# Performance work log

Hardware: AMD Instinct MI355X
Metric: run time of the kernel (lower is better)

Reference implementation:

```python
import jax, jax.numpy as jnp
import numpy as np

NOTES = 51
EMBED = 50
HID = 25
B, T = 512, 2048


def _lstm_layer(x_seq, Wih, Whh, bih, bhh):
    """x_seq: [T, B, in]; returns (ys [T,B,H], h_n [B,H], c_n [B,H]).
    PyTorch gate order: i, f, g, o."""
    H = Whh.shape[1]
    Bsz = x_seq.shape[1]
    # Precompute input projection for all timesteps (one big GEMM).
    xz = jnp.einsum('tbi,gi->tbg', x_seq, Wih) + bih + bhh  # [T, B, 4H]

    def step(carry, xz_t):
        h, c = carry
        z = xz_t + h @ Whh.T  # [B, 4H]
        i, f, g, o = jnp.split(z, 4, axis=-1)
        c = jax.nn.sigmoid(f) * c + jax.nn.sigmoid(i) * jnp.tanh(g)
        h = jax.nn.sigmoid(o) * jnp.tanh(c)
        return (h, c), h

    init = (jnp.zeros((Bsz, H), x_seq.dtype), jnp.zeros((Bsz, H), x_seq.dtype))
    (h_n, c_n), ys = jax.lax.scan(step, init, xz)
    return ys, h_n, c_n


def setup_inputs() -> dict:
    key = jax.random.key(0)
    ks = jax.random.split(key, 12)
    s = 0.1
    inp = {
        'x': jax.random.randint(ks[0], (B, T), 0, NOTES, dtype=jnp.int32),
        'emb': jax.random.normal(ks[1], (NOTES, EMBED), jnp.float32) * s,
        'Wih0': jax.random.normal(ks[2], (4 * HID, EMBED), jnp.float32) * s,
        'Whh0': jax.random.normal(ks[3], (4 * HID, HID), jnp.float32) * s,
        'bih0': jax.random.normal(ks[4], (4 * HID,), jnp.float32) * s,
        'bhh0': jax.random.normal(ks[5], (4 * HID,), jnp.float32) * s,
        'Wih1': jax.random.normal(ks[6], (4 * HID, HID), jnp.float32) * s,
        'Whh1': jax.random.normal(ks[7], (4 * HID, HID), jnp.float32) * s,
        'bih1': jax.random.normal(ks[8], (4 * HID,), jnp.float32) * s,
        'bhh1': jax.random.normal(ks[9], (4 * HID,), jnp.float32) * s,
        'fcW': jax.random.normal(ks[10], (NOTES, HID), jnp.float32) * s,
        'fcb': jax.random.normal(ks[11], (NOTES,), jnp.float32) * s,
    }
    return inp


def reference(x, emb, Wih0, Whh0, bih0, bhh0, Wih1, Whh1, bih1, bhh1, fcW, fcb):
    # Embedding lookup: [B, T, EMBED]
    e = emb[x]
    # batch_first=True -> scan over time: [T, B, EMBED]
    xs = jnp.swapaxes(e, 0, 1)
    y0, h0n, c0n = _lstm_layer(xs, Wih0, Whh0, bih0, bhh0)
    # inter-layer dropout is identity in eval mode
    y1, h1n, c1n = _lstm_layer(y0, Wih1, Whh1, bih1, bhh1)
    out = jnp.swapaxes(y1, 0, 1)  # [B, T, HID]
    # post-LSTM dropout is identity in eval mode
    logits = out @ fcW.T + fcb  # [B, T, NOTES]
    h_n = jnp.stack([h0n, h1n])  # [2, B, HID]
    c_n = jnp.stack([c0n, c1n])
    return (logits, h_n, c_n)
```

## Files before the change

### kernel.cpp

```cpp
#include <hip/hip_runtime.h>

#define T_LEN 2048
#define BATCH 512
#define HID   25
#define NNOTES 51
#define EMBED 50
#define G4    100

typedef float v2f __attribute__((ext_vector_type(2)));

#define REP25(M) M(0) M(1) M(2) M(3) M(4) M(5) M(6) M(7) M(8) M(9) \
  M(10) M(11) M(12) M(13) M(14) M(15) M(16) M(17) M(18) M(19) \
  M(20) M(21) M(22) M(23) M(24)

#define NL2E 1.442695041f

#if __has_builtin(__builtin_amdgcn_exp2f)
#define EXP2(x) __builtin_amdgcn_exp2f(x)
#else
#define EXP2(x) __expf((x) * 0.6931471805599453f)
#endif

__device__ __forceinline__ float bcastf(float v, int lane) {
  return __int_as_float(__builtin_amdgcn_readlane(__float_as_int(v), lane));
}
__device__ __forceinline__ float rcpf_(float x) { return __builtin_amdgcn_rcpf(x); }
__device__ __forceinline__ v2f mk2(float a, float b) { v2f r; r.x = a; r.y = b; return r; }

__device__ __forceinline__ void pin2(v2f& v) { asm volatile("" : "+v"(v)); }
__device__ __forceinline__ void pin1(float& v) { asm volatile("" : "+v"(v)); }

__device__ __forceinline__ void gates(float zA, float zB, float& c, float& h,
                                      float sB, float aB, float bB, int paddr) {
  float uA = rcpf_(1.0f + EXP2(zA * (-NL2E)));
  float eB = EXP2(zB * sB);
  float uB = rcpf_(1.0f + eB);
  float rB = fmaf(aB, uB, bB);
  float sf = __int_as_float(__builtin_amdgcn_ds_bpermute(paddr, __float_as_int(uA)));
  float so = __int_as_float(__builtin_amdgcn_ds_bpermute(paddr, __float_as_int(rB)));
  float cn = fmaf(sf, c, uA * rB);
  c = cn;
  float th = fmaf(2.0f, rcpf_(1.0f + EXP2(cn * (-2.0f * NL2E))), -1.0f);
  h = so * th;
}

__global__ void build_proj(const float* __restrict__ emb,
                           const float* __restrict__ Wih0,
                           const float* __restrict__ bih0,
                           const float* __restrict__ bhh0,
                           float* __restrict__ proj) {
  const int n = blockIdx.x;
  const int j = threadIdx.x;
  if (j < G4) {
    float acc = bih0[j] + bhh0[j];
    #pragma unroll
    for (int e = 0; e < EMBED; ++e)
      acc = fmaf(Wih0[j * EMBED + e], emb[n * EMBED + e], acc);
    proj[n * G4 + j] = acc;
  }
}

__global__ __launch_bounds__(256, 1)
void lstm_seq(
    const int* __restrict__ x, const float* __restrict__ proj,
    const float* __restrict__ Whh0,
    const float* __restrict__ Wih1, const float* __restrict__ Whh1,
    const float* __restrict__ bih1, const float* __restrict__ bhh1,
    const float* __restrict__ fcW, const float* __restrict__ fcb,
    float* __restrict__ out) {
  __shared__ float projL[NNOTES * G4];
  __shared__ int   xL[T_LEN];
  __shared__ float h0Ring[2][32];
  __shared__ v2f   uRing[2][64];
  __shared__ float h1Ring[2][32];

  const int tid = threadIdx.x;
  const int l   = tid & 63;
  const int w   = __builtin_amdgcn_readfirstlane(tid >> 6);
  const int b   = blockIdx.x;

  for (int i = tid; i < NNOTES * G4; i += 256) projL[i] = proj[i];
  const int* xrow = x + b * T_LEN;
  for (int i = tid; i < T_LEN; i += 256) xL[i] = xrow[i];
  __syncthreads();

  const bool act = (l < 50);
  const bool lo  = (l < 25);
  const int jA = act ? l : 0;
  const int jB = act ? (l + 50) : 0;
  const int paddr = ((l + 25) & 63) << 2;

  const float sB = lo ? (-2.0f * NL2E) : (-NL2E);
  const float aB = lo ? 2.0f : 1.0f;
  const float bB = lo ? -1.0f : 0.0f;

  const size_t baseH = (size_t)BATCH * T_LEN * NNOTES;
  const size_t baseC = baseH + (size_t)2 * BATCH * HID;

  if (w == 0) {
    v2f w0[HID];
#define LDW0(i) w0[i] = act ? mk2(Whh0[jA*HID+(i)], Whh0[jB*HID+(i)]) : mk2(0.f,0.f);
    REP25(LDW0)
#undef LDW0
#define PIN0(i) pin2(w0[i]);
    REP25(PIN0)
#undef PIN0

    float h0 = 0.f, c0 = 0.f;
    float h0b[HID];
#define Z0(i) h0b[i] = 0.0f;
    REP25(Z0)
#undef Z0

    int n0 = xL[0];
    v2f xz = mk2(projL[n0 * G4 + jA], projL[n0 * G4 + jB]);

    for (int t = 0; t < T_LEN; ++t) {
      const v2f xzc = xz;
      { const int nn = xL[(t + 1) & (T_LEN - 1)];
        xz = mk2(projL[nn * G4 + jA], projL[nn * G4 + jB]); }

      v2f zp0 = xzc, zp1 = mk2(0.f,0.f), zp2 = mk2(0.f,0.f), zp3 = mk2(0.f,0.f);
#define L0S(i) { const v2f hh = { h0b[i], h0b[i] }; \
      if      (((i)&3)==0) zp0 = __builtin_elementwise_fma(w0[i], hh, zp0); \
      else if (((i)&3)==1) zp1 = __builtin_elementwise_fma(w0[i], hh, zp1); \
      else if (((i)&3)==2) zp2 = __builtin_elementwise_fma(w0[i], hh, zp2); \
      else                 zp3 = __builtin_elementwise_fma(w0[i], hh, zp3); }
      REP25(L0S)
#undef L0S
      const v2f z0 = (zp0 + zp1) + (zp2 + zp3);
      gates(z0.x, z0.y, c0, h0, sB, aB, bB, paddr);
#define BC0(i) h0b[i] = bcastf(h0, i);
      REP25(BC0)
#undef BC0
      if (lo) h0Ring[t & 1][l] = h0;
      __syncthreads();
    }
    __syncthreads();
    __syncthreads();
    __syncthreads();
    if (l < HID) {
      out[baseH + (size_t)b * HID + l] = h0;
      out[baseC + (size_t)b * HID + l] = c0;
    }
  } else if (w == 1) {
    v2f wi1[HID];
#define LDW1(i) wi1[i] = act ? mk2(Wih1[jA*HID+(i)], Wih1[jB*HID+(i)]) : mk2(0.f,0.f);
    REP25(LDW1)
#undef LDW1
    v2f b1 = act ? mk2(bih1[jA] + bhh1[jA], bih1[jB] + bhh1[jB]) : mk2(0.f, 0.f);
#define PIN1(i) pin2(wi1[i]);
    REP25(PIN1)
#undef PIN1
    pin2(b1);

    __syncthreads();
    for (int t = 0; t < T_LEN; ++t) {
      const float hv = h0Ring[t & 1][lo ? l : 0];
      float h0s[HID];
#define BCU(i) h0s[i] = bcastf(hv, i);
      REP25(BCU)
#undef BCU
      v2f u0 = b1, u1 = mk2(0.f,0.f), u2 = mk2(0.f,0.f), u3 = mk2(0.f,0.f);
#define US(i) { const v2f hh = { h0s[i], h0s[i] }; \
      if      (((i)&3)==0) u0 = __builtin_elementwise_fma(wi1[i], hh, u0); \
      else if (((i)&3)==1) u1 = __builtin_elementwise_fma(wi1[i], hh, u1); \
      else if (((i)&3)==2) u2 = __builtin_elementwise_fma(wi1[i], hh, u2); \
      else                 u3 = __builtin_elementwise_fma(wi1[i], hh, u3); }
      REP25(US)
#undef US
      uRing[t & 1][l] = (u0 + u1) + (u2 + u3);
      __syncthreads();
    }
    __syncthreads();
    __syncthreads();
  } else if (w == 2) {
    v2f wh1[HID];
#define LDW2(i) wh1[i] = act ? mk2(Whh1[jA*HID+(i)], Whh1[jB*HID+(i)]) : mk2(0.f,0.f);
    REP25(LDW2)
#undef LDW2
#define PIN2(i) pin2(wh1[i]);
    REP25(PIN2)
#undef PIN2
    float h1 = 0.f, c1 = 0.f;
    float h1b[HID];
#define Z1(i) h1b[i] = 0.0f;
    REP25(Z1)
#undef Z1

    __syncthreads();
    __syncthreads();
    for (int t = 0; t < T_LEN; ++t) {
      const v2f u = uRing[t & 1][l];
      v2f y0 = mk2(0.f,0.f), y1 = mk2(0.f,0.f), y2 = mk2(0.f,0.f), y3 = mk2(0.f,0.f);
#define L1S(i) { const v2f hh = { h1b[i], h1b[i] }; \
      if      (((i)&3)==0) y0 = __builtin_elementwise_fma(wh1[i], hh, y0); \
      else if (((i)&3)==1) y1 = __builtin_elementwise_fma(wh1[i], hh, y1); \
      else if (((i)&3)==2) y2 = __builtin_elementwise_fma(wh1[i], hh, y2); \
      else                 y3 = __builtin_elementwise_fma(wh1[i], hh, y3); }
      REP25(L1S)
#undef L1S
      const v2f z1v = (u + y0) + (y1 + y2) + y3;
      gates(z1v.x, z1v.y, c1, h1, sB, aB, bB, paddr);
#define BC1(i) h1b[i] = bcastf(h1, i);
      REP25(BC1)
#undef BC1
      if (lo) h1Ring[t & 1][l] = h1;
      __syncthreads();
    }
    __syncthreads();
    if (l < HID) {
      out[baseH + (size_t)BATCH * HID + (size_t)b * HID + l] = h1;
      out[baseC + (size_t)BATCH * HID + (size_t)b * HID + l] = c1;
    }
  } else {
    float fcw[HID];
#define LDF(i) fcw[i] = (l < NNOTES) ? fcW[l*HID+(i)] : 0.0f;
    REP25(LDF)
#undef LDF
#define PINF(i) pin1(fcw[i]);
    REP25(PINF)
#undef PINF
    const float fb = (l < NNOTES) ? fcb[l] : 0.0f;
    float* outrow = out + (size_t)b * T_LEN * NNOTES;

    __syncthreads();
    __syncthreads();
    __syncthreads();
    for (int t = 0; t < T_LEN; ++t) {
      const float hv = h1Ring[t & 1][lo ? l : 0];
      float h1s[HID];
#define BCF(i) h1s[i] = bcastf(hv, i);
      REP25(BCF)
#undef BCF
      float a0 = fb, a1 = 0.f, a2 = 0.f, a3 = 0.f;
#define FCS(i) { if      (((i)&3)==0) a0 = fmaf(fcw[i], h1s[i], a0); \
                 else if (((i)&3)==1) a1 = fmaf(fcw[i], h1s[i], a1); \
                 else if (((i)&3)==2) a2 = fmaf(fcw[i], h1s[i], a2); \
                 else                 a3 = fmaf(fcw[i], h1s[i], a3); }
      REP25(FCS)
#undef FCS
      if (l < NNOTES) outrow[t * NNOTES + l] = (a0 + a1) + (a2 + a3);
      asm volatile("s_barrier" ::: "memory");
    }
  }
}

extern "C" void kernel_launch(void* const* d_in, const int* in_sizes, int n_in,
                              void* d_out, int out_size, void* d_ws, size_t ws_size,
                              hipStream_t stream) {
  const int*   x    = (const int*)d_in[0];
  const float* emb  = (const float*)d_in[1];
  const float* Wih0 = (const float*)d_in[2];
  const float* Whh0 = (const float*)d_in[3];
  const float* bih0 = (const float*)d_in[4];
  const float* bhh0 = (const float*)d_in[5];
  const float* Wih1 = (const float*)d_in[6];
  const float* Whh1 = (const float*)d_in[7];
  const float* bih1 = (const float*)d_in[8];
  const float* bhh1 = (const float*)d_in[9];
  const float* fcW  = (const float*)d_in[10];
  const float* fcb  = (const float*)d_in[11];
  float* out  = (float*)d_out;
  float* proj = (float*)d_ws;

  build_proj<<<NNOTES, 128, 0, stream>>>(emb, Wih0, bih0, bhh0, proj);
  lstm_seq<<<BATCH, 256, 0, stream>>>(x, proj, Whh0, Wih1, Whh1, bih1, bhh1,
                                      fcW, fcb, out);
}
```

Measured before the change: 908.1 us.

## Process two batch sequences per block with interleaved recurrences, halving grid size

Each block now handles two batch rows (b and b+256), and every wave runs both independent LSTM chains interleaved, with duplicated accumulators and broadcasts. The grid drops from 512 to 256 blocks, so one resident block per CU covers the whole batch in a single wave instead of two. The two independent dependency chains hide the latency of the serial per-step work, at the cost of more registers and longer per-step instruction sequences.

Measured after the change: 1.207 ms. 1.33x slower.

```diff
diff --git a/kernel.cpp b/kernel.cpp
--- a/kernel.cpp
+++ b/kernel.cpp
@@ -6,6 +6,7 @@
 #define NNOTES 51
 #define EMBED 50
 #define G4    100
+#define NBLK  256
 
 typedef float v2f __attribute__((ext_vector_type(2)));
 
@@ -69,19 +70,22 @@
     const float* __restrict__ fcW, const float* __restrict__ fcb,
     float* __restrict__ out) {
   __shared__ float projL[NNOTES * G4];
-  __shared__ int   xL[T_LEN];
-  __shared__ float h0Ring[2][32];
-  __shared__ v2f   uRing[2][64];
-  __shared__ float h1Ring[2][32];
+  __shared__ int   xL[2][T_LEN];
+  __shared__ float h0Ring[2][2][32];
+  __shared__ v2f   uRing[2][2][64];
+  __shared__ float h1Ring[2][2][32];
 
   const int tid = threadIdx.x;
   const int l   = tid & 63;
   const int w   = __builtin_amdgcn_readfirstlane(tid >> 6);
-  const int b   = blockIdx.x;
+  const int b0  = blockIdx.x;
+  const int b1  = blockIdx.x + NBLK;
 
   for (int i = tid; i < NNOTES * G4; i += 256) projL[i] = proj[i];
-  const int* xrow = x + b * T_LEN;
-  for (int i = tid; i < T_LEN; i += 256) xL[i] = xrow[i];
+  for (int i = tid; i < T_LEN; i += 256) {
+    xL[0][i] = x[b0 * T_LEN + i];
+    xL[1][i] = x[b1 * T_LEN + i];
+  }
   __syncthreads();
 
   const bool act = (l < 50);
@@ -106,70 +110,88 @@
     REP25(PIN0)
 #undef PIN0
 
-    float h0 = 0.f, c0 = 0.f;
-    float h0b[HID];
-#define Z0(i) h0b[i] = 0.0f;
+    float hA = 0.f, cA = 0.f, hB = 0.f, cB = 0.f;
+    float hbA[HID], hbB[HID];
+#define Z0(i) hbA[i] = 0.0f; hbB[i] = 0.0f;
     REP25(Z0)
 #undef Z0
 
-    int n0 = xL[0];
-    v2f xz = mk2(projL[n0 * G4 + jA], projL[n0 * G4 + jB]);
+    v2f x0 = mk2(projL[xL[0][0] * G4 + jA], projL[xL[0][0] * G4 + jB]);
+    v2f x1 = mk2(projL[xL[1][0] * G4 + jA], projL[xL[1][0] * G4 + jB]);
 
     for (int t = 0; t < T_LEN; ++t) {
-      const v2f xzc = xz;
-      { const int nn = xL[(t + 1) & (T_LEN - 1)];
-        xz = mk2(projL[nn * G4 + jA], projL[nn * G4 + jB]); }
-
-      v2f zp0 = xzc, zp1 = mk2(0.f,0.f), zp2 = mk2(0.f,0.f), zp3 = mk2(0.f,0.f);
-#define L0S(i) { const v2f hh = { h0b[i], h0b[i] }; \
-      if      (((i)&3)==0) zp0 = __builtin_elementwise_fma(w0[i], hh, zp0); \
-      else if (((i)&3)==1) zp1 = __builtin_elementwise_fma(w0[i], hh, zp1); \
-      else if (((i)&3)==2) zp2 = __builtin_elementwise_fma(w0[i], hh, zp2); \
-      else                 zp3 = __builtin_elementwise_fma(w0[i], hh, zp3); }
+      const v2f x0c = x0, x1c = x1;
+      { const int nn = (t + 1) & (T_LEN - 1);
+        const int nA = xL[0][nn], nB = xL[1][nn];
+        x0 = mk2(projL[nA * G4 + jA], projL[nA * G4 + jB]);
+        x1 = mk2(projL[nB * G4 + jA], projL[nB * G4 + jB]); }
+
+      v2f zp0 = x0c, zp1 = mk2(0.f,0.f), zp2 = mk2(0.f,0.f), zp3 = mk2(0.f,0.f);
+      v2f zq0 = x1c, zq1 = mk2(0.f,0.f), zq2 = mk2(0.f,0.f), zq3 = mk2(0.f,0.f);
+#define L0S(i) { const v2f ha = { hbA[i], hbA[i] }; const v2f hb = { hbB[i], hbB[i] }; \
+      if      (((i)&3)==0) { zp0 = __builtin_elementwise_fma(w0[i], ha, zp0); \
+                             zq0 = __builtin_elementwise_fma(w0[i], hb, zq0); } \
+      else if (((i)&3)==1) { zp1 = __builtin_elementwise_fma(w0[i], ha, zp1); \
+                             zq1 = __builtin_elementwise_fma(w0[i], hb, zq1); } \
+      else if (((i)&3)==2) { zp2 = __builtin_elementwise_fma(w0[i], ha, zp2); \
+                             zq2 = __builtin_elementwise_fma(w0[i], hb, zq2); } \
+      else                 { zp3 = __builtin_elementwise_fma(w0[i], ha, zp3); \
+                             zq3 = __builtin_elementwise_fma(w0[i], hb, zq3); } }
       REP25(L0S)
 #undef L0S
-      const v2f z0 = (zp0 + zp1) + (zp2 + zp3);
-      gates(z0.x, z0.y, c0, h0, sB, aB, bB, paddr);
-#define BC0(i) h0b[i] = bcastf(h0, i);
+      const v2f zA = (zp0 + zp1) + (zp2 + zp3);
+      const v2f zB = (zq0 + zq1) + (zq2 + zq3);
+      gates(zA.x, zA.y, cA, hA, sB, aB, bB, paddr);
+      gates(zB.x, zB.y, cB, hB, sB, aB, bB, paddr);
+#define BC0(i) hbA[i] = bcastf(hA, i); hbB[i] = bcastf(hB, i);
       REP25(BC0)
 #undef BC0
-      if (lo) h0Ring[t & 1][l] = h0;
+      if (lo) { h0Ring[0][t & 1][l] = hA; h0Ring[1][t & 1][l] = hB; }
       __syncthreads();
     }
     __syncthreads();
     __syncthreads();
     __syncthreads();
     if (l < HID) {
-      out[baseH + (size_t)b * HID + l] = h0;
-      out[baseC + (size_t)b * HID + l] = c0;
+      out[baseH + (size_t)b0 * HID + l] = hA;
+      out[baseH + (size_t)b1 * HID + l] = hB;
+      out[baseC + (size_t)b0 * HID + l] = cA;
+      out[baseC + (size_t)b1 * HID + l] = cB;
     }
   } else if (w == 1) {
     v2f wi1[HID];
 #define LDW1(i) wi1[i] = act ? mk2(Wih1[jA*HID+(i)], Wih1[jB*HID+(i)]) : mk2(0.f,0.f);
     REP25(LDW1)
 #undef LDW1
-    v2f b1 = act ? mk2(bih1[jA] + bhh1[jA], bih1[jB] + bhh1[jB]) : mk2(0.f, 0.f);
+    v2f b1v = act ? mk2(bih1[jA] + bhh1[jA], bih1[jB] + bhh1[jB]) : mk2(0.f, 0.f);
 #define PIN1(i) pin2(wi1[i]);
     REP25(PIN1)
 #undef PIN1
-    pin2(b1);
+    pin2(b1v);
 
     __syncthreads();
     for (int t = 0; t < T_LEN; ++t) {
-      const float hv = h0Ring[t & 1][lo ? l : 0];
-      float h0s[HID];
-#define BCU(i) h0s[i] = bcastf(hv, i);
+      const float hvA = h0Ring[0][t & 1][lo ? l : 0];
+      const float hvB = h0Ring[1][t & 1][lo ? l : 0];
+      float hA[HID], hB[HID];
+#define BCU(i) hA[i] = bcastf(hvA, i); hB[i] = bcastf(hvB, i);
       REP25(BCU)
 #undef BCU
-      v2f u0 = b1, u1 = mk2(0.f,0.f), u2 = mk2(0.f,0.f), u3 = mk2(0.f,0.f);
-#define US(i) { const v2f hh = { h0s[i], h0s[i] }; \
-      if      (((i)&3)==0) u0 = __builtin_elementwise_fma(wi1[i], hh, u0); \
-      else if (((i)&3)==1) u1 = __builtin_elementwise_fma(wi1[i], hh, u1); \
-      else if (((i)&3)==2) u2 = __builtin_elementwise_fma(wi1[i], hh, u2); \
-      else                 u3 = __builtin_elementwise_fma(wi1[i], hh, u3); }
+      v2f a0 = b1v, a1 = mk2(0.f,0.f), a2 = mk2(0.f,0.f), a3 = mk2(0.f,0.f);
+      v2f c0v = b1v, c1v = mk2(0.f,0.f), c2v = mk2(0.f,0.f), c3v = mk2(0.f,0.f);
+#define US(i) { const v2f ha = { hA[i], hA[i] }; const v2f hb = { hB[i], hB[i] }; \
+      if      (((i)&3)==0) { a0 = __builtin_elementwise_fma(wi1[i], ha, a0); \
+                             c0v = __builtin_elementwise_fma(wi1[i], hb, c0v); } \
+      else if (((i)&3)==1) { a1 = __builtin_elementwise_fma(wi1[i], ha, a1); \
+                             c1v = __builtin_elementwise_fma(wi1[i], hb, c1v); } \
+      else if (((i)&3)==2) { a2 = __builtin_elementwise_fma(wi1[i], ha, a2); \
+                             c2v = __builtin_elementwise_fma(wi1[i], hb, c2v); } \
+      else                 { a3 = __builtin_elementwise_fma(wi1[i], ha, a3); \
+                             c3v = __builtin_elementwise_fma(wi1[i], hb, c3v); } }
       REP25(US)
 #undef US
-      uRing[t & 1][l] = (u0 + u1) + (u2 + u3);
+      uRing[0][t & 1][l] = (a0 + a1) + (a2 + a3);
+      uRing[1][t & 1][l] = (c0v + c1v) + (c2v + c3v);
       __syncthreads();
     }
     __syncthreads();
@@ -182,36 +204,46 @@
 #define PIN2(i) pin2(wh1[i]);
     REP25(PIN2)
 #undef PIN2
-    float h1 = 0.f, c1 = 0.f;
-    float h1b[HID];
-#define Z1(i) h1b[i] = 0.0f;
+    float hA = 0.f, cA = 0.f, hB = 0.f, cB = 0.f;
+    float hbA[HID], hbB[HID];
+#define Z1(i) hbA[i] = 0.0f; hbB[i] = 0.0f;
     REP25(Z1)
 #undef Z1
 
     __syncthreads();
     __syncthreads();
     for (int t = 0; t < T_LEN; ++t) {
-      const v2f u = uRing[t & 1][l];
+      const v2f uA = uRing[0][t & 1][l];
+      const v2f uB = uRing[1][t & 1][l];
       v2f y0 = mk2(0.f,0.f), y1 = mk2(0.f,0.f), y2 = mk2(0.f,0.f), y3 = mk2(0.f,0.f);
-#define L1S(i) { const v2f hh = { h1b[i], h1b[i] }; \
-      if      (((i)&3)==0) y0 = __builtin_elementwise_fma(wh1[i], hh, y0); \
-      else if (((i)&3)==1) y1 = __builtin_elementwise_fma(wh1[i], hh, y1); \
-      else if (((i)&3)==2) y2 = __builtin_elementwise_fma(wh1[i], hh, y2); \
-      else                 y3 = __builtin_elementwise_fma(wh1[i], hh, y3); }
+      v2f g0 = mk2(0.f,0.f), g1 = mk2(0.f,0.f), g2 = mk2(0.f,0.f), g3 = mk2(0.f,0.f);
+#define L1S(i) { const v2f ha = { hbA[i], hbA[i] }; const v2f hb = { hbB[i], hbB[i] }; \
+      if      (((i)&3)==0) { y0 = __builtin_elementwise_fma(wh1[i], ha, y0); \
+                             g0 = __builtin_elementwise_fma(wh1[i], hb, g0); } \
+      else if (((i)&3)==1) { y1 = __builtin_elementwise_fma(wh1[i], ha, y1); \
+                             g1 = __builtin_elementwise_fma(wh1[i], hb, g1); } \
+      else if (((i)&3)==2) { y2 = __builtin_elementwise_fma(wh1[i], ha, y2); \
+                             g2 = __builtin_elementwise_fma(wh1[i], hb, g2); } \
+      else                 { y3 = __builtin_elementwise_fma(wh1[i], ha, y3); \
+                             g3 = __builtin_elementwise_fma(wh1[i], hb, g3); } }
       REP25(L1S)
 #undef L1S
-      const v2f z1v = (u + y0) + (y1 + y2) + y3;
-      gates(z1v.x, z1v.y, c1, h1, sB, aB, bB, paddr);
-#define BC1(i) h1b[i] = bcastf(h1, i);
+      const v2f zA = (uA + y0) + (y1 + y2) + y3;
+      const v2f zB = (uB + g0) + (g1 + g2) + g3;
+      gates(zA.x, zA.y, cA, hA, sB, aB, bB, paddr);
+      gates(zB.x, zB.y, cB, hB, sB, aB, bB, paddr);
+#define BC1(i) hbA[i] = bcastf(hA, i); hbB[i] = bcastf(hB, i);
       REP25(BC1)
 #undef BC1
-      if (lo) h1Ring[t & 1][l] = h1;
+      if (lo) { h1Ring[0][t & 1][l] = hA; h1Ring[1][t & 1][l] = hB; }
       __syncthreads();
     }
     __syncthreads();
     if (l < HID) {
-      out[baseH + (size_t)BATCH * HID + (size_t)b * HID + l] = h1;
-      out[baseC + (size_t)BATCH * HID + (size_t)b * HID + l] = c1;
+      out[baseH + (size_t)BATCH * HID + (size_t)b0 * HID + l] = hA;
+      out[baseH + (size_t)BATCH * HID + (size_t)b1 * HID + l] = hB;
+      out[baseC + (size_t)BATCH * HID + (size_t)b0 * HID + l] = cA;
+      out[baseC + (size_t)BATCH * HID + (size_t)b1 * HID + l] = cB;
     }
   } else {
     float fcw[HID];
@@ -222,25 +254,31 @@
     REP25(PINF)
 #undef PINF
     const float fb = (l < NNOTES) ? fcb[l] : 0.0f;
-    float* outrow = out + (size_t)b * T_LEN * NNOTES;
+    float* outrow0 = out + (size_t)b0 * T_LEN * NNOTES;
+    float* outrow1 = out + (size_t)b1 * T_LEN * NNOTES;
 
     __syncthreads();
     __syncthreads();
     __syncthreads();
     for (int t = 0; t < T_LEN; ++t) {
-      const float hv = h1Ring[t & 1][lo ? l : 0];
-      float h1s[HID];
-#define BCF(i) h1s[i] = bcastf(hv, i);
+      const float hvA = h1Ring[0][t & 1][lo ? l : 0];
+      const float hvB = h1Ring[1][t & 1][lo ? l : 0];
+      float hA[HID], hB[HID];
+#define BCF(i) hA[i] = bcastf(hvA, i); hB[i] = bcastf(hvB, i);
       REP25(BCF)
 #undef BCF
       float a0 = fb, a1 = 0.f, a2 = 0.f, a3 = 0.f;
-#define FCS(i) { if      (((i)&3)==0) a0 = fmaf(fcw[i], h1s[i], a0); \
-                 else if (((i)&3)==1) a1 = fmaf(fcw[i], h1s[i], a1); \
-                 else if (((i)&3)==2) a2 = fmaf(fcw[i], h1s[i], a2); \
-                 else                 a3 = fmaf(fcw[i], h1s[i], a3); }
+      float d0 = fb, d1 = 0.f, d2 = 0.f, d3 = 0.f;
+#define FCS(i) { if      (((i)&3)==0) { a0 = fmaf(fcw[i], hA[i], a0); d0 = fmaf(fcw[i], hB[i], d0); } \
+                 else if (((i)&3)==1) { a1 = fmaf(fcw[i], hA[i], a1); d1 = fmaf(fcw[i], hB[i], d1); } \
+                 else if (((i)&3)==2) { a2 = fmaf(fcw[i], hA[i], a2); d2 = fmaf(fcw[i], hB[i], d2); } \
+                 else                 { a3 = fmaf(fcw[i], hA[i], a3); d3 = fmaf(fcw[i], hB[i], d3); } }
       REP25(FCS)
 #undef FCS
-      if (l < NNOTES) outrow[t * NNOTES + l] = (a0 + a1) + (a2 + a3);
+      if (l < NNOTES) {
+        outrow0[t * NNOTES + l] = (a0 + a1) + (a2 + a3);
+        outrow1[t * NNOTES + l] = (d0 + d1) + (d2 + d3);
+      }
       asm volatile("s_barrier" ::: "memory");
     }
   }
@@ -265,6 +303,6 @@
   float* proj = (float*)d_ws;
 
   build_proj<<<NNOTES, 128, 0, stream>>>(emb, Wih0, bih0, bhh0, proj);
-  lstm_seq<<<BATCH, 256, 0, stream>>>(x, proj, Whh0, Wih1, Whh1, bih1, bhh1,
-                                      fcW, fcb, out);
-}
+  lstm_seq<<<NBLK, 256, 0, stream>>>(x, proj, Whh0, Wih1, Whh1, bih1, bhh1,
+                                     fcW, fcb, out);
+}
```
